# Kernel optimization log

Hardware: AMD Instinct MI355X
Metric: run time of the kernel (lower is better)

The kernel has to match this reference:

```python
import jax, jax.numpy as jnp
import numpy as np

N_NODES = 50000


def binarize(w):
    # straight-through sign binarization (forward: sign, backward: identity)
    return w + jax.lax.stop_gradient(jnp.sign(w) - w)


def sage_conv(x, src, dst, w_l, b_l, w_r, num_nodes):
    # PyG SAGEConv with mean aggregation:
    # out[i] = lin_l(mean_{j in N(i)} x[j]) + lin_r(x[i])
    msgs = x[src]  # [E, F] gather from source nodes
    agg = jax.ops.segment_sum(msgs, dst, num_segments=num_nodes)  # [N, F]
    deg = jax.ops.segment_sum(jnp.ones_like(dst, dtype=x.dtype), dst,
                              num_segments=num_nodes)
    agg = agg / jnp.maximum(deg, 1.0)[:, None]
    return agg @ w_l.T + b_l + x @ w_r.T


def setup_inputs() -> dict:
    key = jax.random.key(0)
    ks = jax.random.split(key, 9)
    in_dim, hid, out_dim = 96, 128, 64
    x = jax.random.normal(ks[0], (N_NODES, in_dim), dtype=jnp.float32)
    edge_index = jax.random.randint(ks[1], (2, 800000), 0, N_NODES, dtype=jnp.int64)
    s1 = 1.0 / np.sqrt(in_dim)
    s2 = 1.0 / np.sqrt(hid)
    w1_l = jax.random.uniform(ks[2], (hid, in_dim), minval=-s1, maxval=s1)
    b1 = jax.random.uniform(ks[3], (hid,), minval=-s1, maxval=s1)
    w1_r = jax.random.uniform(ks[4], (hid, in_dim), minval=-s1, maxval=s1)
    w2_l = jax.random.uniform(ks[5], (out_dim, hid), minval=-s2, maxval=s2)
    b2 = jax.random.uniform(ks[6], (out_dim,), minval=-s2, maxval=s2)
    w2_r = jax.random.uniform(ks[7], (out_dim, hid), minval=-s2, maxval=s2)
    return {"x": x, "edge_index": edge_index, "w1_l": w1_l, "b1": b1,
            "w1_r": w1_r, "w2_l": w2_l, "b2": b2, "w2_r": w2_r}


def reference(x, edge_index, w1_l, b1, w1_r, w2_l, b2, w2_r):
    src, dst = edge_index[0], edge_index[1]
    h = sage_conv(x, src, dst, binarize(w1_l), b1, binarize(w1_r), N_NODES)
    h = jax.nn.relu(h)
    out = sage_conv(h, src, dst, binarize(w2_l), b2, binarize(w2_r), N_NODES)
    return jnp.squeeze(out, axis=-1) if out.shape[-1] == 1 else out
```

## Files before the change

### kernel.cpp

```cpp
#include <hip/hip_runtime.h>
#include <cstdint>
#include <cstddef>


#define N_NODES 50000
#define IN_DIM 96
#define HID 128
#define OUT_DIM 64
#define DCAP 64
#define BKT_SHIFT 7
#define BKT_SZ 128
#define CAP 3072
#define NBMAX 392

typedef __attribute__((ext_vector_type(8))) short bf16x8;
typedef __attribute__((ext_vector_type(4))) float f32x4;

static inline size_t alignUp(size_t v, size_t a) { return (v + a - 1) & ~(a - 1); }

__device__ __forceinline__ uint16_t f2bf(float f) {
  uint32_t u = __float_as_uint(f);
  return (uint16_t)((u + 0x7FFF + ((u >> 16) & 1)) >> 16);
}
__device__ __forceinline__ float bflo(uint32_t v) { return __uint_as_float(v << 16); }
__device__ __forceinline__ float bfhi(uint32_t v) { return __uint_as_float(v & 0xFFFF0000u); }

__device__ __forceinline__ uint16_t sgnbf(float w) {
  return (w > 0.f) ? (uint16_t)0x3F80 : ((w < 0.f) ? (uint16_t)0xBF80 : (uint16_t)0);
}

#define NS1 (128 * 192)
#define NS2 (128 * 128)
#define SCAT_CHUNK 2048

__global__ __launch_bounds__(256) void scatter_prep_kernel(
    const int* __restrict__ src, const int* __restrict__ dst,
    int* __restrict__ bucketCursor, uint32_t* __restrict__ bucketBuf,
    int E, int nScat, int NB,
    const float* __restrict__ x,
    const float* __restrict__ w1l, const float* __restrict__ w1r,
    const float* __restrict__ w2l, const float* __restrict__ w2r,
    uint16_t* __restrict__ S1t, uint16_t* __restrict__ S2t,
    uint16_t* __restrict__ xb, int total4) {
  __shared__ uint32_t stage[SCAT_CHUNK];
  __shared__ int h[NBMAX];
  __shared__ int g[NBMAX];
  __shared__ int c[NBMAX];
  const int t = threadIdx.x;
  if ((int)blockIdx.x < nScat) {
    const int base = blockIdx.x * SCAT_CHUNK;
    const int end = min(base + SCAT_CHUNK, E);
    for (int b = t; b < NBMAX; b += 256) h[b] = 0;
    __syncthreads();
    for (int i = base + t; i < end; i += 256) {
      const uint32_t d = (uint32_t)dst[i];
      stage[i - base] = (uint32_t)src[i] | (d << 16);
      atomicAdd(&h[d >> BKT_SHIFT], 1);
    }
    __syncthreads();
    for (int b = t; b < NB; b += 256) {
      if (h[b]) g[b] = b * CAP + atomicAdd(&bucketCursor[b], h[b]);
      c[b] = 0;
    }
    __syncthreads();
    const int m = end - base;
    for (int i = t; i < m; i += 256) {
      const uint32_t pack = stage[i];
      const int b = (int)(pack >> (16 + BKT_SHIFT));
      const int ticket = atomicAdd(&c[b], 1);
      bucketBuf[g[b] + ticket] = pack;
    }
  } else {
    const int idx = ((int)blockIdx.x - nScat) * 256 + t;
    if (idx < NS1) {
      int n = idx / 192, k = idx - n * 192;
      float w = (k < 96) ? w1l[n * 96 + k] : w1r[n * 96 + (k - 96)];
      S1t[idx] = sgnbf(w);
    } else if (idx < NS1 + NS2) {
      int i2 = idx - NS1;
      int n = i2 >> 7, k = i2 & 127;
      float w = (n < 64) ? w2l[n * 128 + k] : w2r[(n - 64) * 128 + k];
      S2t[i2] = sgnbf(w);
    } else {
      int i = idx - NS1 - NS2;
      if (i < total4) {
        float4 v = *(const float4*)(x + (size_t)i * 4);
        uint32_t p0 = (uint32_t)f2bf(v.x) | ((uint32_t)f2bf(v.y) << 16);
        uint32_t p1 = (uint32_t)f2bf(v.z) | ((uint32_t)f2bf(v.w) << 16);
        *(uint2*)(xb + (size_t)i * 4) = make_uint2(p0, p1);
      }
    }
  }
}

__global__ __launch_bounds__(256) void bucket_build_kernel(const uint32_t* __restrict__ bucketBuf,
    const int* __restrict__ bucketCursor, int* __restrict__ cnt,
    uint16_t* __restrict__ adj16, int N) {
  __shared__ int h[BKT_SZ];
  __shared__ int cur[BKT_SZ];
  const int t = threadIdx.x;
  const int b = blockIdx.x;
  const int nodeBase = b << BKT_SHIFT;
  const int beg = b * CAP;
  const int m = min(bucketCursor[b], CAP);
  if (t < BKT_SZ) { h[t] = 0; cur[t] = 0; }
  __syncthreads();
  for (int i = t; i < m; i += 256)
    atomicAdd(&h[(bucketBuf[beg + i] >> 16) & (BKT_SZ - 1)], 1);
  __syncthreads();
  const int node = nodeBase + t;
  if (t < BKT_SZ && node < N) cnt[node] = h[t];
  for (int i = t; i < m; i += 256) {
    const uint32_t u = bucketBuf[beg + i];
    const int ld = (int)((u >> 16) & (BKT_SZ - 1));
    const int ticket = atomicAdd(&cur[ld], 1);
    if (ticket < DCAP)
      adj16[((size_t)(nodeBase + ld) << 6) + ticket] = (uint16_t)(u & 0xFFFFu);
  }
}

__global__ __launch_bounds__(256) void agg1_kernel(const uint16_t* __restrict__ xb,
    const uint16_t* __restrict__ adj16, const int* __restrict__ cnt,
    uint16_t* __restrict__ AGGb, int nNodes) {
  const int sg = threadIdx.x >> 4;
  const int j = threadIdx.x & 15;
  const int n = blockIdx.x * 16 + sg;
  if (n >= nNodes) return;
  const int deg = min(cnt[n], DCAP);
  const int beg = n << 6;
  const int end = beg + deg;
  const bool act = j < 12;
  const int foff = j * 8;
  float a0 = 0.f, a1 = 0.f, a2 = 0.f, a3 = 0.f, a4 = 0.f, a5 = 0.f, a6 = 0.f, a7 = 0.f;

  int e = beg;
  for (; e + 8 <= end; e += 8) {
    const uint4 av = *(const uint4*)(adj16 + e);
    const uint32_t s0 = av.x & 0xFFFFu, s1 = av.x >> 16;
    const uint32_t s2 = av.y & 0xFFFFu, s3 = av.y >> 16;
    const uint32_t s4 = av.z & 0xFFFFu, s5 = av.z >> 16;
    const uint32_t s6 = av.w & 0xFFFFu, s7 = av.w >> 16;
    uint4 v0 = make_uint4(0u,0u,0u,0u), v1 = v0, v2 = v0, v3 = v0;
    uint4 v4 = v0, v5 = v0, v6 = v0, v7 = v0;
    if (act) {
      v0 = *(const uint4*)(xb + (size_t)s0 * IN_DIM + foff);
      v1 = *(const uint4*)(xb + (size_t)s1 * IN_DIM + foff);
      v2 = *(const uint4*)(xb + (size_t)s2 * IN_DIM + foff);
      v3 = *(const uint4*)(xb + (size_t)s3 * IN_DIM + foff);
      v4 = *(const uint4*)(xb + (size_t)s4 * IN_DIM + foff);
      v5 = *(const uint4*)(xb + (size_t)s5 * IN_DIM + foff);
      v6 = *(const uint4*)(xb + (size_t)s6 * IN_DIM + foff);
      v7 = *(const uint4*)(xb + (size_t)s7 * IN_DIM + foff);
    }
    __builtin_amdgcn_sched_barrier(0);
    a0 += (bflo(v0.x) + bflo(v1.x) + bflo(v2.x) + bflo(v3.x)) + (bflo(v4.x) + bflo(v5.x) + bflo(v6.x) + bflo(v7.x));
    a1 += (bfhi(v0.x) + bfhi(v1.x) + bfhi(v2.x) + bfhi(v3.x)) + (bfhi(v4.x) + bfhi(v5.x) + bfhi(v6.x) + bfhi(v7.x));
    a2 += (bflo(v0.y) + bflo(v1.y) + bflo(v2.y) + bflo(v3.y)) + (bflo(v4.y) + bflo(v5.y) + bflo(v6.y) + bflo(v7.y));
    a3 += (bfhi(v0.y) + bfhi(v1.y) + bfhi(v2.y) + bfhi(v3.y)) + (bfhi(v4.y) + bfhi(v5.y) + bfhi(v6.y) + bfhi(v7.y));
    a4 += (bflo(v0.z) + bflo(v1.z) + bflo(v2.z) + bflo(v3.z)) + (bflo(v4.z) + bflo(v5.z) + bflo(v6.z) + bflo(v7.z));
    a5 += (bfhi(v0.z) + bfhi(v1.z) + bfhi(v2.z) + bfhi(v3.z)) + (bfhi(v4.z) + bfhi(v5.z) + bfhi(v6.z) + bfhi(v7.z));
    a6 += (bflo(v0.w) + bflo(v1.w) + bflo(v2.w) + bflo(v3.w)) + (bflo(v4.w) + bflo(v5.w) + bflo(v6.w) + bflo(v7.w));
    a7 += (bfhi(v0.w) + bfhi(v1.w) + bfhi(v2.w) + bfhi(v3.w)) + (bfhi(v4.w) + bfhi(v5.w) + bfhi(v6.w) + bfhi(v7.w));
  }
  if (e + 4 <= end) {
    const uint2 av = *(const uint2*)(adj16 + e);
    const uint32_t s0 = av.x & 0xFFFFu, s1 = av.x >> 16;
    const uint32_t s2 = av.y & 0xFFFFu, s3 = av.y >> 16;
    uint4 v0 = make_uint4(0u,0u,0u,0u), v1 = v0, v2 = v0, v3 = v0;
    if (act) {
      v0 = *(const uint4*)(xb + (size_t)s0 * IN_DIM + foff);
      v1 = *(const uint4*)(xb + (size_t)s1 * IN_DIM + foff);
      v2 = *(const uint4*)(xb + (size_t)s2 * IN_DIM + foff);
      v3 = *(const uint4*)(xb + (size_t)s3 * IN_DIM + foff);
    }
    __builtin_amdgcn_sched_barrier(0);
    a0 += bflo(v0.x) + bflo(v1.x) + bflo(v2.x) + bflo(v3.x);
    a1 += bfhi(v0.x) + bfhi(v1.x) + bfhi(v2.x) + bfhi(v3.x);
    a2 += bflo(v0.y) + bflo(v1.y) + bflo(v2.y) + bflo(v3.y);
    a3 += bfhi(v0.y) + bfhi(v1.y) + bfhi(v2.y) + bfhi(v3.y);
    a4 += bflo(v0.z) + bflo(v1.z) + bflo(v2.z) + bflo(v3.z);
    a5 += bfhi(v0.z) + bfhi(v1.z) + bfhi(v2.z) + bfhi(v3.z);
    a6 += bflo(v0.w) + bflo(v1.w) + bflo(v2.w) + bflo(v3.w);
    a7 += bfhi(v0.w) + bfhi(v1.w) + bfhi(v2.w) + bfhi(v3.w);
    e += 4;
  }
  for (; e < end; ++e) {
    const uint32_t s = adj16[e];
    uint4 v = make_uint4(0u,0u,0u,0u);
    if (act) v = *(const uint4*)(xb + (size_t)s * IN_DIM + foff);
    a0 += bflo(v.x); a1 += bfhi(v.x);
    a2 += bflo(v.y); a3 += bfhi(v.y);
    a4 += bflo(v.z); a5 += bfhi(v.z);
    a6 += bflo(v.w); a7 += bfhi(v.w);
  }
  if (act) {
    const float inv = 1.0f / (float)(deg > 1 ? deg : 1);
    uint4 o;
    o.x = (uint32_t)f2bf(a0 * inv) | ((uint32_t)f2bf(a1 * inv) << 16);
    o.y = (uint32_t)f2bf(a2 * inv) | ((uint32_t)f2bf(a3 * inv) << 16);
    o.z = (uint32_t)f2bf(a4 * inv) | ((uint32_t)f2bf(a5 * inv) << 16);
    o.w = (uint32_t)f2bf(a6 * inv) | ((uint32_t)f2bf(a7 * inv) << 16);
    *(uint4*)(AGGb + (size_t)n * IN_DIM + foff) = o;
  }
}

__global__ __launch_bounds__(256) void final_kernel(const uint16_t* __restrict__ T2b,
    const float* __restrict__ R2, const uint16_t* __restrict__ adj16,
    const int* __restrict__ cnt, float* __restrict__ out, int nNodes) {
  const int sg = threadIdx.x >> 4;
  const int j = threadIdx.x & 15;
  const int n = blockIdx.x * 16 + sg;
  if (n >= nNodes) return;
  const int deg = min(cnt[n], DCAP);
  const int beg = n << 6;
  const int end = beg + deg;
  const int foff = j * 4;
  float a0 = 0.f, a1 = 0.f, a2 = 0.f, a3 = 0.f;

  int e = beg;
  for (; e + 8 <= end; e += 8) {
    const uint4 av = *(const uint4*)(adj16 + e);
    const uint32_t s0 = av.x & 0xFFFFu, s1 = av.x >> 16;
    const uint32_t s2 = av.y & 0xFFFFu, s3 = av.y >> 16;
    const uint32_t s4 = av.z & 0xFFFFu, s5 = av.z >> 16;
    const uint32_t s6 = av.w & 0xFFFFu, s7 = av.w >> 16;
    const uint2 v0 = *(const uint2*)(T2b + (size_t)s0 * 64 + foff);
    const uint2 v1 = *(const uint2*)(T2b + (size_t)s1 * 64 + foff);
    const uint2 v2 = *(const uint2*)(T2b + (size_t)s2 * 64 + foff);
    const uint2 v3 = *(const uint2*)(T2b + (size_t)s3 * 64 + foff);
    const uint2 v4 = *(const uint2*)(T2b + (size_t)s4 * 64 + foff);
    const uint2 v5 = *(const uint2*)(T2b + (size_t)s5 * 64 + foff);
    const uint2 v6 = *(const uint2*)(T2b + (size_t)s6 * 64 + foff);
    const uint2 v7 = *(const uint2*)(T2b + (size_t)s7 * 64 + foff);
    __builtin_amdgcn_sched_barrier(0);
    a0 += (bflo(v0.x) + bflo(v1.x) + bflo(v2.x) + bflo(v3.x)) + (bflo(v4.x) + bflo(v5.x) + bflo(v6.x) + bflo(v7.x));
    a1 += (bfhi(v0.x) + bfhi(v1.x) + bfhi(v2.x) + bfhi(v3.x)) + (bfhi(v4.x) + bfhi(v5.x) + bfhi(v6.x) + bfhi(v7.x));
    a2 += (bflo(v0.y) + bflo(v1.y) + bflo(v2.y) + bflo(v3.y)) + (bflo(v4.y) + bflo(v5.y) + bflo(v6.y) + bflo(v7.y));
    a3 += (bfhi(v0.y) + bfhi(v1.y) + bfhi(v2.y) + bfhi(v3.y)) + (bfhi(v4.y) + bfhi(v5.y) + bfhi(v6.y) + bfhi(v7.y));
  }
  if (e + 4 <= end) {
    const uint2 av = *(const uint2*)(adj16 + e);
    const uint32_t s0 = av.x & 0xFFFFu, s1 = av.x >> 16;
    const uint32_t s2 = av.y & 0xFFFFu, s3 = av.y >> 16;
    const uint2 v0 = *(const uint2*)(T2b + (size_t)s0 * 64 + foff);
    const uint2 v1 = *(const uint2*)(T2b + (size_t)s1 * 64 + foff);
    const uint2 v2 = *(const uint2*)(T2b + (size_t)s2 * 64 + foff);
    const uint2 v3 = *(const uint2*)(T2b + (size_t)s3 * 64 + foff);
    __builtin_amdgcn_sched_barrier(0);
    a0 += bflo(v0.x) + bflo(v1.x) + bflo(v2.x) + bflo(v3.x);
    a1 += bfhi(v0.x) + bfhi(v1.x) + bfhi(v2.x) + bfhi(v3.x);
    a2 += bflo(v0.y) + bflo(v1.y) + bflo(v2.y) + bflo(v3.y);
    a3 += bfhi(v0.y) + bfhi(v1.y) + bfhi(v2.y) + bfhi(v3.y);
    e += 4;
  }
  for (; e < end; ++e) {
    const uint32_t s = adj16[e];
    const uint2 v = *(const uint2*)(T2b + (size_t)s * 64 + foff);
    a0 += bflo(v.x); a1 += bfhi(v.x);
    a2 += bflo(v.y); a3 += bfhi(v.y);
  }
  const float inv = 1.0f / (float)(deg > 1 ? deg : 1);
  const float4 r = *(const float4*)(R2 + (size_t)n * 64 + foff);
  float4 o;
  o.x = a0 * inv + r.x;
  o.y = a1 * inv + r.y;
  o.z = a2 * inv + r.z;
  o.w = a3 * inv + r.w;
  *(float4*)(out + (size_t)n * 64 + foff) = o;
}

#define SP1 200
#define SP2 136
#define HP 136
__global__ __launch_bounds__(256) void gemm12_kernel(
    const uint16_t* __restrict__ AGGb, const uint16_t* __restrict__ xb,
    const uint16_t* __restrict__ S1t, const uint16_t* __restrict__ S2t,
    const float* __restrict__ b1, const float* __restrict__ b2,
    uint16_t* __restrict__ T2b, float* __restrict__ R2, int M) {
  __shared__ uint16_t BS[128 * SP1];
  __shared__ uint16_t Hs[64 * HP];
  const int tid = threadIdx.x;
  const int wv = tid >> 6;
  const int lane = tid & 63;
  const int m16 = lane & 15;
  const int quad = lane >> 4;
  const int rowBase = blockIdx.x * 64 + wv * 16;
  int arow = rowBase + m16;
  if (arow >= M) arow = M - 1;
  const int kq = quad * 8;

#pragma unroll
  for (int i = 0; i < 12; ++i) {
    const int idx8 = tid + i * 256;
    const int col = idx8 / 24;
    const int k8 = (idx8 - col * 24) * 8;
    const bf16x8 v = *(const bf16x8*)(S1t + (size_t)idx8 * 8);
    *(bf16x8*)&BS[col * SP1 + k8] = v;
  }
  bf16x8 a1f[6];
#pragma unroll
  for (int s = 0; s < 3; ++s)
    a1f[s] = *(const bf16x8*)(AGGb + (size_t)arow * IN_DIM + s * 32 + kq);
#pragma unroll
  for (int s = 0; s < 3; ++s)
    a1f[3 + s] = *(const bf16x8*)(xb + (size_t)arow * IN_DIM + s * 32 + kq);
  __syncthreads();

  f32x4 acc1[8];
#pragma unroll
  for (int cf = 0; cf < 8; ++cf) acc1[cf] = (f32x4){0.f, 0.f, 0.f, 0.f};
#pragma unroll
  for (int s = 0; s < 6; ++s) {
#pragma unroll
    for (int cf = 0; cf < 8; ++cf) {
      const bf16x8 b = *(const bf16x8*)&BS[(cf * 16 + m16) * SP1 + s * 32 + kq];
      acc1[cf] = __builtin_amdgcn_mfma_f32_16x16x32_bf16(a1f[s], b, acc1[cf], 0, 0, 0);
    }
  }

#pragma unroll
  for (int cf = 0; cf < 8; ++cf) {
    const int col = cf * 16 + m16;
    const float bias = b1[col];
#pragma unroll
    for (int r = 0; r < 4; ++r) {
      const float v = fmaxf(acc1[cf][r] + bias, 0.f);
      Hs[(wv * 16 + quad * 4 + r) * HP + col] = f2bf(v);
    }
  }
  __syncthreads();

#pragma unroll
  for (int i = 0; i < 8; ++i) {
    const int idx8 = tid + i * 256;
    const int col = idx8 >> 4;
    const int k8 = (idx8 & 15) * 8;
    const bf16x8 v = *(const bf16x8*)(S2t + (size_t)idx8 * 8);
    *(bf16x8*)&BS[col * SP2 + k8] = v;
  }
  __syncthreads();

  f32x4 acc2[8];
#pragma unroll
  for (int cf = 0; cf < 8; ++cf) acc2[cf] = (f32x4){0.f, 0.f, 0.f, 0.f};
#pragma unroll
  for (int s = 0; s < 4; ++s) {
    const bf16x8 a = *(const bf16x8*)&Hs[(wv * 16 + m16) * HP + s * 32 + kq];
#pragma unroll
    for (int cf = 0; cf < 8; ++cf) {
      const bf16x8 b = *(const bf16x8*)&BS[(cf * 16 + m16) * SP2 + s * 32 + kq];
      acc2[cf] = __builtin_amdgcn_mfma_f32_16x16x32_bf16(a, b, acc2[cf], 0, 0, 0);
    }
  }

#pragma unroll
  for (int cf = 0; cf < 8; ++cf) {
    const int col = cf * 16 + m16;
#pragma unroll
    for (int r = 0; r < 4; ++r) {
      const int row = rowBase + quad * 4 + r;
      if (row < M) {
        const float v = acc2[cf][r];
        if (col < 64) {
          T2b[(size_t)row * 64 + col] = f2bf(v);
        } else {
          R2[(size_t)row * 64 + (col - 64)] = v + b2[col - 64];
        }
      }
    }
  }
}

extern "C" void kernel_launch(void* const* d_in, const int* in_sizes, int n_in,
                              void* d_out, int out_size, void* d_ws, size_t ws_size,
                              hipStream_t stream) {
  const float* x   = (const float*)d_in[0];
  const int*   ei  = (const int*)d_in[1];
  const float* w1l = (const float*)d_in[2];
  const float* b1  = (const float*)d_in[3];
  const float* w1r = (const float*)d_in[4];
  const float* w2l = (const float*)d_in[5];
  const float* b2  = (const float*)d_in[6];
  const float* w2r = (const float*)d_in[7];
  float* out = (float*)d_out;

  const int N = in_sizes[0] / IN_DIM;
  const int E = in_sizes[1] / 2;
  const int* src = ei;
  const int* dst = ei + E;
  const int NB = (N + BKT_SZ - 1) >> BKT_SHIFT;

  char* p = (char*)d_ws;
  uint16_t* AGGb = (uint16_t*)p; p += alignUp((size_t)N * IN_DIM * sizeof(uint16_t), 256);
  uint16_t* T2b  = (uint16_t*)p; p += alignUp((size_t)N * 64 * sizeof(uint16_t), 256);
  float* R2      = (float*)p;    p += alignUp((size_t)N * 64 * sizeof(float), 256);
  uint16_t* xb = (uint16_t*)p; p += alignUp((size_t)N * IN_DIM * sizeof(uint16_t), 256);
  uint16_t* S1t = (uint16_t*)p; p += alignUp(NS1 * sizeof(uint16_t), 256);
  uint16_t* S2t = (uint16_t*)p; p += alignUp(NS2 * sizeof(uint16_t), 256);
  uint16_t* adj16 = (uint16_t*)p; p += alignUp((size_t)N * DCAP * sizeof(uint16_t), 256);
  int* cnt = (int*)p; p += alignUp((size_t)N * sizeof(int), 256);
  uint32_t* bucketBuf = (uint32_t*)p; p += alignUp((size_t)NBMAX * CAP * sizeof(uint32_t), 256);
  int* bucketCursor = (int*)p; p += alignUp(NBMAX * sizeof(int), 256);
  (void)ws_size; (void)n_in; (void)out_size;

  hipMemsetAsync(bucketCursor, 0, NBMAX * sizeof(int), stream);

  const int nScat = (E + SCAT_CHUNK - 1) / SCAT_CHUNK;
  const int total4 = N * IN_DIM / 4;
  const int prepThreads = NS1 + NS2 + total4;
  const int nPrep = (prepThreads + 255) / 256;
  scatter_prep_kernel<<<nScat + nPrep, 256, 0, stream>>>(
      src, dst, bucketCursor, bucketBuf, E, nScat, NB,
      x, w1l, w1r, w2l, w2r, S1t, S2t, xb, total4);

  bucket_build_kernel<<<NB, 256, 0, stream>>>(bucketBuf, bucketCursor, cnt, adj16, N);

  const int nodeBlocks16 = (N + 15) / 16;
  agg1_kernel<<<nodeBlocks16, 256, 0, stream>>>(xb, adj16, cnt, AGGb, N);

  const int gemmBlocks = (N + 63) / 64;
  gemm12_kernel<<<gemmBlocks, 256, 0, stream>>>(AGGb, xb, S1t, S2t, b1, b2, T2b, R2, N);

  final_kernel<<<nodeBlocks16, 256, 0, stream>>>(T2b, R2, adj16, cnt, out, N);
}
```

Baseline: 166.9 us.

## Fuse layer-1 neighbor aggregation into the GEMM kernel's A-fragment construction

Merges the separate aggregation kernel into the two-layer GEMM kernel. Each lane gathers its node's neighbor features directly into the MFMA A-fragment layout (4 lanes per row, 3 strided uint4 loads per neighbor), so the AGGb intermediate buffer and one kernel launch go away. The cost is that the gather now runs inside a large-LDS GEMM block with fewer nodes per block and more registers per lane. Occupancy and latency hiding for the irregular gathers may suffer, and the load on each wave depends on degree imbalance across its 16 rows.

After: 170.5 us. 2.2% more time.

```diff
diff --git a/kernel.cpp b/kernel.cpp
--- a/kernel.cpp
+++ b/kernel.cpp
@@ -119,88 +119,146 @@
   }
 }
 
-__global__ __launch_bounds__(256) void agg1_kernel(const uint16_t* __restrict__ xb,
+#define SP1 200
+#define SP2 136
+#define HP 136
+__global__ __launch_bounds__(256) void gemm_agg_kernel(
+    const uint16_t* __restrict__ xb,
     const uint16_t* __restrict__ adj16, const int* __restrict__ cnt,
-    uint16_t* __restrict__ AGGb, int nNodes) {
-  const int sg = threadIdx.x >> 4;
-  const int j = threadIdx.x & 15;
-  const int n = blockIdx.x * 16 + sg;
-  if (n >= nNodes) return;
-  const int deg = min(cnt[n], DCAP);
-  const int beg = n << 6;
-  const int end = beg + deg;
-  const bool act = j < 12;
-  const int foff = j * 8;
-  float a0 = 0.f, a1 = 0.f, a2 = 0.f, a3 = 0.f, a4 = 0.f, a5 = 0.f, a6 = 0.f, a7 = 0.f;
-
-  int e = beg;
-  for (; e + 8 <= end; e += 8) {
-    const uint4 av = *(const uint4*)(adj16 + e);
+    const uint16_t* __restrict__ S1t, const uint16_t* __restrict__ S2t,
+    const float* __restrict__ b1, const float* __restrict__ b2,
+    uint16_t* __restrict__ T2b, float* __restrict__ R2, int M) {
+  __shared__ uint16_t BS[128 * SP1];
+  __shared__ uint16_t Hs[64 * HP];
+  const int tid = threadIdx.x;
+  const int wv = tid >> 6;
+  const int lane = tid & 63;
+  const int m16 = lane & 15;
+  const int quad = lane >> 4;
+  const int rowBase = blockIdx.x * 64 + wv * 16;
+  int arow = rowBase + m16;
+  if (arow >= M) arow = M - 1;
+  const int kq = quad * 8;
+
+#pragma unroll
+  for (int i = 0; i < 12; ++i) {
+    const int idx8 = tid + i * 256;
+    const int col = idx8 / 24;
+    const int k8 = (idx8 - col * 24) * 8;
+    const bf16x8 v = *(const bf16x8*)(S1t + (size_t)idx8 * 8);
+    *(bf16x8*)&BS[col * SP1 + k8] = v;
+  }
+
+  const int deg = min(cnt[arow], DCAP);
+  const uint16_t* adjRow = adj16 + ((size_t)arow << 6);
+  const uint16_t* xq = xb + kq;
+  float g0[8], g1[8], g2[8];
+#pragma unroll
+  for (int k = 0; k < 8; ++k) { g0[k] = 0.f; g1[k] = 0.f; g2[k] = 0.f; }
+
+#define ACC8(A, W) { A[0] += bflo(W.x); A[1] += bfhi(W.x); A[2] += bflo(W.y); A[3] += bfhi(W.y); \
+                     A[4] += bflo(W.z); A[5] += bfhi(W.z); A[6] += bflo(W.w); A[7] += bfhi(W.w); }
+  int e = 0;
+  for (; e + 4 <= deg; e += 4) {
+    const uint2 av = *(const uint2*)(adjRow + e);
     const uint32_t s0 = av.x & 0xFFFFu, s1 = av.x >> 16;
     const uint32_t s2 = av.y & 0xFFFFu, s3 = av.y >> 16;
-    const uint32_t s4 = av.z & 0xFFFFu, s5 = av.z >> 16;
-    const uint32_t s6 = av.w & 0xFFFFu, s7 = av.w >> 16;
-    uint4 v0 = make_uint4(0u,0u,0u,0u), v1 = v0, v2 = v0, v3 = v0;
-    uint4 v4 = v0, v5 = v0, v6 = v0, v7 = v0;
-    if (act) {
-      v0 = *(const uint4*)(xb + (size_t)s0 * IN_DIM + foff);
-      v1 = *(const uint4*)(xb + (size_t)s1 * IN_DIM + foff);
-      v2 = *(const uint4*)(xb + (size_t)s2 * IN_DIM + foff);
-      v3 = *(const uint4*)(xb + (size_t)s3 * IN_DIM + foff);
-      v4 = *(const uint4*)(xb + (size_t)s4 * IN_DIM + foff);
-      v5 = *(const uint4*)(xb + (size_t)s5 * IN_DIM + foff);
-      v6 = *(const uint4*)(xb + (size_t)s6 * IN_DIM + foff);
-      v7 = *(const uint4*)(xb + (size_t)s7 * IN_DIM + foff);
-    }
+    const uint16_t* p0 = xq + (size_t)s0 * IN_DIM;
+    const uint16_t* p1 = xq + (size_t)s1 * IN_DIM;
+    const uint16_t* p2 = xq + (size_t)s2 * IN_DIM;
+    const uint16_t* p3 = xq + (size_t)s3 * IN_DIM;
+    const uint4 w00 = *(const uint4*)(p0), w01 = *(const uint4*)(p0 + 32), w02 = *(const uint4*)(p0 + 64);
+    const uint4 w10 = *(const uint4*)(p1), w11 = *(const uint4*)(p1 + 32), w12 = *(const uint4*)(p1 + 64);
+    const uint4 w20 = *(const uint4*)(p2), w21 = *(const uint4*)(p2 + 32), w22 = *(const uint4*)(p2 + 64);
+    const uint4 w30 = *(const uint4*)(p3), w31 = *(const uint4*)(p3 + 32), w32 = *(const uint4*)(p3 + 64);
     __builtin_amdgcn_sched_barrier(0);
-    a0 += (bflo(v0.x) + bflo(v1.x) + bflo(v2.x) + bflo(v3.x)) + (bflo(v4.x) + bflo(v5.x) + bflo(v6.x) + bflo(v7.x));
-    a1 += (bfhi(v0.x) + bfhi(v1.x) + bfhi(v2.x) + bfhi(v3.x)) + (bfhi(v4.x) + bfhi(v5.x) + bfhi(v6.x) + bfhi(v7.x));
-    a2 += (bflo(v0.y) + bflo(v1.y) + bflo(v2.y) + bflo(v3.y)) + (bflo(v4.y) + bflo(v5.y) + bflo(v6.y) + bflo(v7.y));
-    a3 += (bfhi(v0.y) + bfhi(v1.y) + bfhi(v2.y) + bfhi(v3.y)) + (bfhi(v4.y) + bfhi(v5.y) + bfhi(v6.y) + bfhi(v7.y));
-    a4 += (bflo(v0.z) + bflo(v1.z) + bflo(v2.z) + bflo(v3.z)) + (bflo(v4.z) + bflo(v5.z) + bflo(v6.z) + bflo(v7.z));
-    a5 += (bfhi(v0.z) + bfhi(v1.z) + bfhi(v2.z) + bfhi(v3.z)) + (bfhi(v4.z) + bfhi(v5.z) + bfhi(v6.z) + bfhi(v7.z));
-    a6 += (bflo(v0.w) + bflo(v1.w) + bflo(v2.w) + bflo(v3.w)) + (bflo(v4.w) + bflo(v5.w) + bflo(v6.w) + bflo(v7.w));
-    a7 += (bfhi(v0.w) + bfhi(v1.w) + bfhi(v2.w) + bfhi(v3.w)) + (bfhi(v4.w) + bfhi(v5.w) + bfhi(v6.w) + bfhi(v7.w));
-  }
-  if (e + 4 <= end) {
-    const uint2 av = *(const uint2*)(adj16 + e);
-    const uint32_t s0 = av.x & 0xFFFFu, s1 = av.x >> 16;
-    const uint32_t s2 = av.y & 0xFFFFu, s3 = av.y >> 16;
-    uint4 v0 = make_uint4(0u,0u,0u,0u), v1 = v0, v2 = v0, v3 = v0;
-    if (act) {
-      v0 = *(const uint4*)(xb + (size_t)s0 * IN_DIM + foff);
-      v1 = *(const uint4*)(xb + (size_t)s1 * IN_DIM + foff);
-      v2 = *(const uint4*)(xb + (size_t)s2 * IN_DIM + foff);
-      v3 = *(const uint4*)(xb + (size_t)s3 * IN_DIM + foff);
-    }
-    __builtin_amdgcn_sched_barrier(0);
-    a0 += bflo(v0.x) + bflo(v1.x) + bflo(v2.x) + bflo(v3.x);
-    a1 += bfhi(v0.x) + bfhi(v1.x) + bfhi(v2.x) + bfhi(v3.x);
-    a2 += bflo(v0.y) + bflo(v1.y) + bflo(v2.y) + bflo(v3.y);
-    a3 += bfhi(v0.y) + bfhi(v1.y) + bfhi(v2.y) + bfhi(v3.y);
-    a4 += bflo(v0.z) + bflo(v1.z) + bflo(v2.z) + bflo(v3.z);
-    a5 += bfhi(v0.z) + bfhi(v1.z) + bfhi(v2.z) + bfhi(v3.z);
-    a6 += bflo(v0.w) + bflo(v1.w) + bflo(v2.w) + bflo(v3.w);
-    a7 += bfhi(v0.w) + bfhi(v1.w) + bfhi(v2.w) + bfhi(v3.w);
-    e += 4;
-  }
-  for (; e < end; ++e) {
-    const uint32_t s = adj16[e];
-    uint4 v = make_uint4(0u,0u,0u,0u);
-    if (act) v = *(const uint4*)(xb + (size_t)s * IN_DIM + foff);
-    a0 += bflo(v.x); a1 += bfhi(v.x);
-    a2 += bflo(v.y); a3 += bfhi(v.y);
-    a4 += bflo(v.z); a5 += bfhi(v.z);
-    a6 += bflo(v.w); a7 += bfhi(v.w);
-  }
-  if (act) {
-    const float inv = 1.0f / (float)(deg > 1 ? deg : 1);
-    uint4 o;
-    o.x = (uint32_t)f2bf(a0 * inv) | ((uint32_t)f2bf(a1 * inv) << 16);
-    o.y = (uint32_t)f2bf(a2 * inv) | ((uint32_t)f2bf(a3 * inv) << 16);
-    o.z = (uint32_t)f2bf(a4 * inv) | ((uint32_t)f2bf(a5 * inv) << 16);
-    o.w = (uint32_t)f2bf(a6 * inv) | ((uint32_t)f2bf(a7 * inv) << 16);
-    *(uint4*)(AGGb + (size_t)n * IN_DIM + foff) = o;
+    ACC8(g0, w00); ACC8(g0, w10); ACC8(g0, w20); ACC8(g0, w30);
+    ACC8(g1, w01); ACC8(g1, w11); ACC8(g1, w21); ACC8(g1, w31);
+    ACC8(g2, w02); ACC8(g2, w12); ACC8(g2, w22); ACC8(g2, w32);
+  }
+  for (; e < deg; ++e) {
+    const uint32_t s = adjRow[e];
+    const uint16_t* p = xq + (size_t)s * IN_DIM;
+    const uint4 w0 = *(const uint4*)(p), w1 = *(const uint4*)(p + 32), w2 = *(const uint4*)(p + 64);
+    ACC8(g0, w0); ACC8(g1, w1); ACC8(g2, w2);
+  }
+#undef ACC8
+
+  const float inv = 1.0f / (float)(deg > 1 ? deg : 1);
+  bf16x8 a1f[6];
+#pragma unroll
+  for (int k = 0; k < 8; ++k) {
+    a1f[0][k] = (short)f2bf(g0[k] * inv);
+    a1f[1][k] = (short)f2bf(g1[k] * inv);
+    a1f[2][k] = (short)f2bf(g2[k] * inv);
+  }
+#pragma unroll
+  for (int s = 0; s < 3; ++s)
+    a1f[3 + s] = *(const bf16x8*)(xb + (size_t)arow * IN_DIM + s * 32 + kq);
+  __syncthreads();
+
+  f32x4 acc1[8];
+#pragma unroll
+  for (int cf = 0; cf < 8; ++cf) acc1[cf] = (f32x4){0.f, 0.f, 0.f, 0.f};
+#pragma unroll
+  for (int s = 0; s < 6; ++s) {
+#pragma unroll
+    for (int cf = 0; cf < 8; ++cf) {
+      const bf16x8 b = *(const bf16x8*)&BS[(cf * 16 + m16) * SP1 + s * 32 + kq];
+      acc1[cf] = __builtin_amdgcn_mfma_f32_16x16x32_bf16(a1f[s], b, acc1[cf], 0, 0, 0);
+    }
+  }
+
+#pragma unroll
+  for (int cf = 0; cf < 8; ++cf) {
+    const int col = cf * 16 + m16;
+    const float bias = b1[col];
+#pragma unroll
+    for (int r = 0; r < 4; ++r) {
+      const float v = fmaxf(acc1[cf][r] + bias, 0.f);
+      Hs[(wv * 16 + quad * 4 + r) * HP + col] = f2bf(v);
+    }
+  }
+  __syncthreads();
+
+#pragma unroll
+  for (int i = 0; i < 8; ++i) {
+    const int idx8 = tid + i * 256;
+    const int col = idx8 >> 4;
+    const int k8 = (idx8 & 15) * 8;
+    const bf16x8 v = *(const bf16x8*)(S2t + (size_t)idx8 * 8);
+    *(bf16x8*)&BS[col * SP2 + k8] = v;
+  }
+  __syncthreads();
+
+  f32x4 acc2[8];
+#pragma unroll
+  for (int cf = 0; cf < 8; ++cf) acc2[cf] = (f32x4){0.f, 0.f, 0.f, 0.f};
+#pragma unroll
+  for (int s = 0; s < 4; ++s) {
+    const bf16x8 a = *(const bf16x8*)&Hs[(wv * 16 + m16) * HP + s * 32 + kq];
+#pragma unroll
+    for (int cf = 0; cf < 8; ++cf) {
+      const bf16x8 b = *(const bf16x8*)&BS[(cf * 16 + m16) * SP2 + s * 32 + kq];
+      acc2[cf] = __builtin_amdgcn_mfma_f32_16x16x32_bf16(a, b, acc2[cf], 0, 0, 0);
+    }
+  }
+
+#pragma unroll
+  for (int cf = 0; cf < 8; ++cf) {
+    const int col = cf * 16 + m16;
+#pragma unroll
+    for (int r = 0; r < 4; ++r) {
+      const int row = rowBase + quad * 4 + r;
+      if (row < M) {
+        const float v = acc2[cf][r];
+        if (col < 64) {
+          T2b[(size_t)row * 64 + col] = f2bf(v);
+        } else {
+          R2[(size_t)row * 64 + (col - 64)] = v + b2[col - 64];
+        }
+      }
+    }
   }
 }
 
@@ -269,108 +327,6 @@
   *(float4*)(out + (size_t)n * 64 + foff) = o;
 }
 
-#define SP1 200
-#define SP2 136
-#define HP 136
-__global__ __launch_bounds__(256) void gemm12_kernel(
-    const uint16_t* __restrict__ AGGb, const uint16_t* __restrict__ xb,
-    const uint16_t* __restrict__ S1t, const uint16_t* __restrict__ S2t,
-    const float* __restrict__ b1, const float* __restrict__ b2,
-    uint16_t* __restrict__ T2b, float* __restrict__ R2, int M) {
-  __shared__ uint16_t BS[128 * SP1];
-  __shared__ uint16_t Hs[64 * HP];
-  const int tid = threadIdx.x;
-  const int wv = tid >> 6;
-  const int lane = tid & 63;
-  const int m16 = lane & 15;
-  const int quad = lane >> 4;
-  const int rowBase = blockIdx.x * 64 + wv * 16;
-  int arow = rowBase + m16;
-  if (arow >= M) arow = M - 1;
-  const int kq = quad * 8;
-
-#pragma unroll
-  for (int i = 0; i < 12; ++i) {
-    const int idx8 = tid + i * 256;
-    const int col = idx8 / 24;
-    const int k8 = (idx8 - col * 24) * 8;
-    const bf16x8 v = *(const bf16x8*)(S1t + (size_t)idx8 * 8);
-    *(bf16x8*)&BS[col * SP1 + k8] = v;
-  }
-  bf16x8 a1f[6];
-#pragma unroll
-  for (int s = 0; s < 3; ++s)
-    a1f[s] = *(const bf16x8*)(AGGb + (size_t)arow * IN_DIM + s * 32 + kq);
-#pragma unroll
-  for (int s = 0; s < 3; ++s)
-    a1f[3 + s] = *(const bf16x8*)(xb + (size_t)arow * IN_DIM + s * 32 + kq);
-  __syncthreads();
-
-  f32x4 acc1[8];
-#pragma unroll
-  for (int cf = 0; cf < 8; ++cf) acc1[cf] = (f32x4){0.f, 0.f, 0.f, 0.f};
-#pragma unroll
-  for (int s = 0; s < 6; ++s) {
-#pragma unroll
-    for (int cf = 0; cf < 8; ++cf) {
-      const bf16x8 b = *(const bf16x8*)&BS[(cf * 16 + m16) * SP1 + s * 32 + kq];
-      acc1[cf] = __builtin_amdgcn_mfma_f32_16x16x32_bf16(a1f[s], b, acc1[cf], 0, 0, 0);
-    }
-  }
-
-#pragma unroll
-  for (int cf = 0; cf < 8; ++cf) {
-    const int col = cf * 16 + m16;
-    const float bias = b1[col];
-#pragma unroll
-    for (int r = 0; r < 4; ++r) {
-      const float v = fmaxf(acc1[cf][r] + bias, 0.f);
-      Hs[(wv * 16 + quad * 4 + r) * HP + col] = f2bf(v);
-    }
-  }
-  __syncthreads();
-
-#pragma unroll
-  for (int i = 0; i < 8; ++i) {
-    const int idx8 = tid + i * 256;
-    const int col = idx8 >> 4;
-    const int k8 = (idx8 & 15) * 8;
-    const bf16x8 v = *(const bf16x8*)(S2t + (size_t)idx8 * 8);
-    *(bf16x8*)&BS[col * SP2 + k8] = v;
-  }
-  __syncthreads();
-
-  f32x4 acc2[8];
-#pragma unroll
-  for (int cf = 0; cf < 8; ++cf) acc2[cf] = (f32x4){0.f, 0.f, 0.f, 0.f};
-#pragma unroll
-  for (int s = 0; s < 4; ++s) {
-    const bf16x8 a = *(const bf16x8*)&Hs[(wv * 16 + m16) * HP + s * 32 + kq];
-#pragma unroll
-    for (int cf = 0; cf < 8; ++cf) {
-      const bf16x8 b = *(const bf16x8*)&BS[(cf * 16 + m16) * SP2 + s * 32 + kq];
-      acc2[cf] = __builtin_amdgcn_mfma_f32_16x16x32_bf16(a, b, acc2[cf], 0, 0, 0);
-    }
-  }
-
-#pragma unroll
-  for (int cf = 0; cf < 8; ++cf) {
-    const int col = cf * 16 + m16;
-#pragma unroll
-    for (int r = 0; r < 4; ++r) {
-      const int row = rowBase + quad * 4 + r;
-      if (row < M) {
-        const float v = acc2[cf][r];
-        if (col < 64) {
-          T2b[(size_t)row * 64 + col] = f2bf(v);
-        } else {
-          R2[(size_t)row * 64 + (col - 64)] = v + b2[col - 64];
-        }
-      }
-    }
-  }
-}
-
 extern "C" void kernel_launch(void* const* d_in, const int* in_sizes, int n_in,
                               void* d_out, int out_size, void* d_ws, size_t ws_size,
                               hipStream_t stream) {
@@ -391,7 +347,6 @@
   const int NB = (N + BKT_SZ - 1) >> BKT_SHIFT;
 
   char* p = (char*)d_ws;
-  uint16_t* AGGb = (uint16_t*)p; p += alignUp((size_t)N * IN_DIM * sizeof(uint16_t), 256);
   uint16_t* T2b  = (uint16_t*)p; p += alignUp((size_t)N * 64 * sizeof(uint16_t), 256);
   float* R2      = (float*)p;    p += alignUp((size_t)N * 64 * sizeof(float), 256);
   uint16_t* xb = (uint16_t*)p; p += alignUp((size_t)N * IN_DIM * sizeof(uint16_t), 256);
@@ -415,11 +370,9 @@
 
   bucket_build_kernel<<<NB, 256, 0, stream>>>(bucketBuf, bucketCursor, cnt, adj16, N);
 
+  const int gemmBlocks = (N + 63) / 64;
+  gemm_agg_kernel<<<gemmBlocks, 256, 0, stream>>>(xb, adj16, cnt, S1t, S2t, b1, b2, T2b, R2, N);
+
   const int nodeBlocks16 = (N + 15) / 16;
-  agg1_kernel<<<nodeBlocks16, 256, 0, stream>>>(xb, adj16, cnt, AGGb, N);
-
-  const int gemmBlocks = (N + 63) / 64;
-  gemm12_kernel<<<gemmBlocks, 256, 0, stream>>>(AGGb, xb, S1t, S2t, b1, b2, T2b, R2, N);
-
   final_kernel<<<nodeBlocks16, 256, 0, stream>>>(T2b, R2, adj16, cnt, out, N);
 }
```
